# Optimization experiments

Measured on AMD Instinct MI355X. Metric: run time of the kernel, lower is better.

Reference implementation:

```python
import jax, jax.numpy as jnp
import numpy as np

N = 100000   # nodes
E = 1600000  # edges
D = 128      # input feature dim
H1, H2 = 128, 128    # GCN hidden sizes
M1, M2 = 256, 128    # MLP hidden sizes
BN_EPS = 1e-5


def setup_inputs() -> dict:
    key = jax.random.key(0)
    ks = jax.random.split(key, 20)
    x = jax.random.normal(ks[0], (N, D), dtype=jnp.float32)
    edge_index = jax.random.randint(ks[1], (2, E), 0, N, dtype=jnp.int32)

    def lin(k, fi, fo):
        s = 1.0 / np.sqrt(fi)
        return jax.random.uniform(k, (fi, fo), jnp.float32, -s, s)

    inp = {"x": x, "edge_index": edge_index}
    inp["Wg1"] = lin(ks[2], D, H1);  inp["bg1"] = jnp.zeros((H1,), jnp.float32)
    inp["g1"]  = jnp.ones((H1,), jnp.float32); inp["be1"] = jnp.zeros((H1,), jnp.float32)
    inp["Wg2"] = lin(ks[3], H1, H2); inp["bg2"] = jnp.zeros((H2,), jnp.float32)
    inp["g2"]  = jnp.ones((H2,), jnp.float32); inp["be2"] = jnp.zeros((H2,), jnp.float32)
    inp["Wm1"] = lin(ks[4], H2, M1); inp["bm1"] = jnp.zeros((M1,), jnp.float32)
    inp["g3"]  = jnp.ones((M1,), jnp.float32); inp["be3"] = jnp.zeros((M1,), jnp.float32)
    inp["Wm2"] = lin(ks[5], M1, M2); inp["bm2"] = jnp.zeros((M2,), jnp.float32)
    inp["g4"]  = jnp.ones((M2,), jnp.float32); inp["be4"] = jnp.zeros((M2,), jnp.float32)
    inp["Wo"]  = lin(ks[6], M2, 1);  inp["bo"]  = jnp.zeros((1,), jnp.float32)
    return inp


def batch_norm(x, gamma, beta):
    # training-mode BatchNorm1d over the node/batch axis, biased variance
    mean = jnp.mean(x, axis=0)
    var = jnp.mean((x - mean) ** 2, axis=0)
    return (x - mean) * jax.lax.rsqrt(var + BN_EPS) * gamma + beta


def gcn_conv(x, src, dst, W, b):
    # PyG GCNConv: add self-loops, sym-normalize, aggregate (xW) over edges
    h = x @ W                                              # [N, F_out]
    deg = jnp.zeros((N,), x.dtype).at[dst].add(1.0) + 1.0  # in-degree + self-loop
    dinv = jax.lax.rsqrt(deg)
    coef = (dinv[src] * dinv[dst])[:, None]                # [E, 1]
    agg = jax.ops.segment_sum(h[src] * coef, dst, num_segments=N)
    agg = agg + h * (dinv * dinv)[:, None]                 # self-loop term
    return agg + b


def reference(x, edge_index, Wg1, bg1, g1, be1, Wg2, bg2, g2, be2,
              Wm1, bm1, g3, be3, Wm2, bm2, g4, be4, Wo, bo):
    src, dst = edge_index[0], edge_index[1]
    # GCN blocks: relu(dropout(bn(conv(x)))); dropout is identity in eval
    h = jax.nn.relu(batch_norm(gcn_conv(x, src, dst, Wg1, bg1), g1, be1))
    h = jax.nn.relu(batch_norm(gcn_conv(h, src, dst, Wg2, bg2), g2, be2))
    # MLP blocks
    h = jax.nn.relu(batch_norm(h @ Wm1 + bm1, g3, be3))
    h = jax.nn.relu(batch_norm(h @ Wm2 + bm2, g4, be4))
    return jax.nn.sigmoid(h @ Wo + bo)
```

## Files before the change

kernel.cpp:

```cpp
#include <hip/hip_runtime.h>
#include <hip/hip_bf16.h>
#include <math.h>


typedef __attribute__((ext_vector_type(8))) short bf16x8;
typedef __attribute__((ext_vector_type(4))) float f32x4;

__device__ inline void split_bf16(float x, ushort& h, ushort& l) {
    union { float f; unsigned u; } a; a.f = x;
    unsigned r = (a.u + 0x7FFFu + ((a.u >> 16) & 1u)) >> 16;
    h = (ushort)r;
    union { unsigned u; float f; } hb; hb.u = r << 16;
    float lo = x - hb.f;
    union { float f; unsigned u; } b; b.f = lo;
    unsigned r2 = (b.u + 0x7FFFu + ((b.u >> 16) & 1u)) >> 16;
    l = (ushort)r2;
}

__global__ void degree_kernel(const int* __restrict__ dst, int* __restrict__ deg, int E) {
    int i = blockIdx.x * blockDim.x + threadIdx.x;
    if (i < E) atomicAdd(&deg[dst[i]], 1);
}

__global__ void dinv_kernel(const int* __restrict__ deg, float* __restrict__ dinv, int N) {
    int i = blockIdx.x * blockDim.x + threadIdx.x;
    if (i < N) dinv[i] = rsqrtf((float)(deg[i] + 1));
}

__global__ void blocksum_kernel(const int* __restrict__ deg, int* __restrict__ bsum, int N) {
    __shared__ int sh[256];
    int tid = threadIdx.x;
    int base = blockIdx.x * 1024 + tid * 4;
    int s = 0;
    #pragma unroll
    for (int j = 0; j < 4; ++j) { int idx = base + j; if (idx < N) s += deg[idx]; }
    sh[tid] = s; __syncthreads();
    for (int off = 128; off > 0; off >>= 1) {
        if (tid < off) sh[tid] += sh[tid + off];
        __syncthreads();
    }
    if (tid == 0) bsum[blockIdx.x] = sh[0];
}

__global__ void scan_bsum_kernel(int* bsum, int nb) {
    if (threadIdx.x == 0 && blockIdx.x == 0) {
        int run = 0;
        for (int i = 0; i < nb; ++i) { int v = bsum[i]; bsum[i] = run; run += v; }
    }
}

__global__ void scanwrite_kernel(const int* __restrict__ deg, const int* __restrict__ bsumex,
                                 int* __restrict__ row_ptr, int* __restrict__ cursor,
                                 int N, int Etot) {
    __shared__ int sh[256];
    int tid = threadIdx.x;
    int base = blockIdx.x * 1024 + tid * 4;
    int v[4]; int tsum = 0;
    #pragma unroll
    for (int j = 0; j < 4; ++j) { int idx = base + j; v[j] = (idx < N) ? deg[idx] : 0; tsum += v[j]; }
    sh[tid] = tsum; __syncthreads();
    for (int off = 1; off < 256; off <<= 1) {
        int x = (tid >= off) ? sh[tid - off] : 0;
        __syncthreads();
        sh[tid] += x;
        __syncthreads();
    }
    int run = sh[tid] - tsum + bsumex[blockIdx.x];
    #pragma unroll
    for (int j = 0; j < 4; ++j) {
        int idx = base + j;
        if (idx < N) { row_ptr[idx] = run; cursor[idx] = run; }
        run += v[j];
    }
    if (blockIdx.x == 0 && tid == 0) row_ptr[N] = Etot;
}

__global__ void scatter_kernel(const int* __restrict__ src, const int* __restrict__ dst,
                               int* __restrict__ cursor, int* __restrict__ edge_src, int E) {
    int i = blockIdx.x * blockDim.x + threadIdx.x;
    if (i < E) {
        int d = dst[i];
        int pos = atomicAdd(&cursor[d], 1);
        edge_src[pos] = src[i];
    }
}

__global__ void wsplit_kernel(const float* __restrict__ W, ushort* __restrict__ Wh,
                              ushort* __restrict__ Wl, int K, int FO) {
    int t = blockIdx.x * 256 + threadIdx.x;
    if (t >= K * FO) return;
    int j   = t & 7;
    int ci  = (t >> 3) & 127;
    int rest = t >> 10;
    int nkg = K >> 3;
    int kg  = rest % nkg;
    int cb  = rest / nkg;
    float w = W[(size_t)(kg * 8 + j) * FO + cb * 128 + ci];
    ushort h, l; split_bf16(w, h, l);
    Wh[t] = h; Wl[t] = l;
}

#define AIDX(kg, r, j) ((kg) * 1032 + (r) * 8 + (j))

template<bool ACT>
__global__ __launch_bounds__(256)
void gemm_mfma_kernel(const float* __restrict__ A, const ushort* __restrict__ W2h,
                      const ushort* __restrict__ W2l, float* __restrict__ C,
                      int nrows, int K, int FO,
                      const float* __restrict__ scale, const float* __restrict__ shift)
{
    __shared__ ushort AsH[4 * 1032 + 8];
    __shared__ ushort AsL[4 * 1032 + 8];
    const int tid  = threadIdx.x;
    const int lane = tid & 63;
    const int wid  = tid >> 6;
    const int wm   = wid & 1, wn = wid >> 1;
    const int row0 = blockIdx.x * 128;
    const int cb   = blockIdx.y;
    const int c0   = cb * 128;
    const int nkg  = K >> 3;
    const int l15  = lane & 15;
    const int l4   = lane >> 4;

    f32x4 zero = {0.f, 0.f, 0.f, 0.f};
    f32x4 acc[4][4];
    #pragma unroll
    for (int m = 0; m < 4; ++m)
        #pragma unroll
        for (int n = 0; n < 4; ++n) acc[m][n] = zero;

    for (int k0 = 0; k0 < K; k0 += 32) {
        #pragma unroll
        for (int p = 0; p < 4; ++p) {
            int q  = p * 256 + tid;
            int r  = q >> 3;
            int kq = (q & 7) * 4;
            int gr = row0 + r;
            float4 v = make_float4(0.f, 0.f, 0.f, 0.f);
            if (gr < nrows) {
                v = *(const float4*)&A[(size_t)gr * K + k0 + kq];
                if (ACT) {
                    float4 sc = *(const float4*)&scale[k0 + kq];
                    float4 sf = *(const float4*)&shift[k0 + kq];
                    v.x = fmaxf(fmaf(v.x, sc.x, sf.x), 0.f);
                    v.y = fmaxf(fmaf(v.y, sc.y, sf.y), 0.f);
                    v.z = fmaxf(fmaf(v.z, sc.z, sf.z), 0.f);
                    v.w = fmaxf(fmaf(v.w, sc.w, sf.w), 0.f);
                }
            }
            ushort h[4], l[4];
            split_bf16(v.x, h[0], l[0]); split_bf16(v.y, h[1], l[1]);
            split_bf16(v.z, h[2], l[2]); split_bf16(v.w, h[3], l[3]);
            int idx = AIDX(kq >> 3, r, kq & 7);
            union { uint2 u; ushort s[4]; } ph, pl;
            ph.s[0] = h[0]; ph.s[1] = h[1]; ph.s[2] = h[2]; ph.s[3] = h[3];
            pl.s[0] = l[0]; pl.s[1] = l[1]; pl.s[2] = l[2]; pl.s[3] = l[3];
            *(uint2*)&AsH[idx] = ph.u;
            *(uint2*)&AsL[idx] = pl.u;
        }
        __syncthreads();

        const int kgbase = k0 >> 3;
        bf16x8 bh[4], bl[4];
        #pragma unroll
        for (int n = 0; n < 4; ++n) {
            int ci = wn * 64 + n * 16 + l15;
            size_t off = (((size_t)(cb * nkg + kgbase + l4)) * 128 + ci) * 8;
            bh[n] = *(const bf16x8*)&W2h[off];
            bl[n] = *(const bf16x8*)&W2l[off];
        }
        bf16x8 ah[4], al[4];
        #pragma unroll
        for (int m = 0; m < 4; ++m) {
            int idx = AIDX(l4, wm * 64 + m * 16 + l15, 0);
            ah[m] = *(const bf16x8*)&AsH[idx];
            al[m] = *(const bf16x8*)&AsL[idx];
        }
        #pragma unroll
        for (int m = 0; m < 4; ++m)
            #pragma unroll
            for (int n = 0; n < 4; ++n) {
                acc[m][n] = __builtin_amdgcn_mfma_f32_16x16x32_bf16(ah[m], bh[n], acc[m][n], 0, 0, 0);
                acc[m][n] = __builtin_amdgcn_mfma_f32_16x16x32_bf16(ah[m], bl[n], acc[m][n], 0, 0, 0);
                acc[m][n] = __builtin_amdgcn_mfma_f32_16x16x32_bf16(al[m], bh[n], acc[m][n], 0, 0, 0);
            }
        __syncthreads();
    }

    #pragma unroll
    for (int m = 0; m < 4; ++m) {
        int rbase = row0 + wm * 64 + m * 16 + l4 * 4;
        #pragma unroll
        for (int r = 0; r < 4; ++r) {
            int gr = rbase + r;
            if (gr < nrows) {
                #pragma unroll
                for (int n = 0; n < 4; ++n) {
                    int gc = c0 + wn * 64 + n * 16 + l15;
                    C[(size_t)gr * FO + gc] = acc[m][n][r];
                }
            }
        }
    }
}

__global__ void agg_kernel(const float* __restrict__ T, float* __restrict__ Aout,
                           const float* __restrict__ dinv,
                           const int* __restrict__ row_ptr, const int* __restrict__ edge_src,
                           int nrows)
{
    int gw = (blockIdx.x * blockDim.x + threadIdx.x) >> 6;
    int lane = threadIdx.x & 63;
    int nw = (gridDim.x * blockDim.x) >> 6;
    int c = lane * 2;
    for (int i = gw; i < nrows; i += nw) {
        float di = dinv[i];
        int e0 = row_ptr[i], e1 = row_ptr[i + 1];
        float ax = 0.f, ay = 0.f;
        for (int ch = e0; ch < e1; ch += 64) {
            int rem = e1 - ch;
            int es = i; float w = 0.f;
            if (lane < rem) { es = edge_src[ch + lane]; w = dinv[es]; }
            int cnt = min(rem, 64);
            int rcnt = (cnt + 3) & ~3;
            for (int j = 0; j < rcnt; j += 4) {
                int   s0 = __shfl(es, j),     s1 = __shfl(es, j + 1);
                int   s2 = __shfl(es, j + 2), s3 = __shfl(es, j + 3);
                float w0 = __shfl(w, j),      w1 = __shfl(w, j + 1);
                float w2 = __shfl(w, j + 2),  w3 = __shfl(w, j + 3);
                float2 v0 = *(const float2*)&T[(size_t)s0 * 128 + c];
                float2 v1 = *(const float2*)&T[(size_t)s1 * 128 + c];
                float2 v2 = *(const float2*)&T[(size_t)s2 * 128 + c];
                float2 v3 = *(const float2*)&T[(size_t)s3 * 128 + c];
                ax = fmaf(w0, v0.x, ax); ay = fmaf(w0, v0.y, ay);
                ax = fmaf(w1, v1.x, ax); ay = fmaf(w1, v1.y, ay);
                ax = fmaf(w2, v2.x, ax); ay = fmaf(w2, v2.y, ay);
                ax = fmaf(w3, v3.x, ax); ay = fmaf(w3, v3.y, ay);
            }
        }
        float2 self = *(const float2*)&T[(size_t)i * 128 + c];
        float2 o;
        o.x = fmaf(di, ax, di * di * self.x);
        o.y = fmaf(di, ay, di * di * self.y);
        *(float2*)&Aout[(size_t)i * 128 + c] = o;
    }
}

__global__ void colstats_kernel(const float* __restrict__ X, int nrows, int F, int rpb,
                                float* __restrict__ colsum, float* __restrict__ colsq)
{
    __shared__ float ss[256], sq[256];
    int tid = threadIdx.x;
    int c = tid & (F - 1);
    int roff = tid / F;
    int rstep = 256 / F;
    int r0 = blockIdx.x * rpb;
    int r1 = min(nrows, r0 + rpb);
    float s = 0.f, q = 0.f;
    for (int r = r0 + roff; r < r1; r += rstep) {
        float v = X[(size_t)r * F + c];
        s += v; q += v * v;
    }
    ss[tid] = s; sq[tid] = q;
    __syncthreads();
    if (tid < F) {
        float S = ss[tid], Q = sq[tid];
        for (int k = tid + F; k < 256; k += F) { S += ss[k]; Q += sq[k]; }
        atomicAdd(&colsum[tid], S);
        atomicAdd(&colsq[tid], Q);
    }
}

__global__ void bnparam_kernel(const float* __restrict__ colsum, const float* __restrict__ colsq,
                               const float* __restrict__ g, const float* __restrict__ be,
                               float* __restrict__ scale, float* __restrict__ shift,
                               int F, float invN)
{
    int c = blockIdx.x * blockDim.x + threadIdx.x;
    if (c < F) {
        float mean = colsum[c] * invN;
        float var = colsq[c] * invN - mean * mean;
        float rs = rsqrtf(var + 1e-5f);
        float sc = g[c] * rs;
        scale[c] = sc;
        shift[c] = be[c] - mean * sc;
    }
}

__global__ void final_kernel(const float* __restrict__ A, const float* __restrict__ Wo,
                             const float* __restrict__ bo,
                             const float* __restrict__ scale, const float* __restrict__ shift,
                             float* __restrict__ out, int nrows)
{
    int gw = (blockIdx.x * blockDim.x + threadIdx.x) >> 6;
    int lane = threadIdx.x & 63;
    int nw = (gridDim.x * blockDim.x) >> 6;
    int c = lane * 2;
    float2 w = *(const float2*)&Wo[c];
    float2 sc = *(const float2*)&scale[c];
    float2 sf = *(const float2*)&shift[c];
    float bias = bo[0];
    for (int i = gw; i < nrows; i += nw) {
        float2 v = *(const float2*)&A[(size_t)i * 128 + c];
        float x = fmaxf(fmaf(v.x, sc.x, sf.x), 0.f) * w.x
                + fmaxf(fmaf(v.y, sc.y, sf.y), 0.f) * w.y;
        #pragma unroll
        for (int off = 32; off > 0; off >>= 1) x += __shfl_down(x, off);
        if (lane == 0) out[i] = 1.f / (1.f + expf(-(x + bias)));
    }
}

extern "C" void kernel_launch(void* const* d_in, const int* in_sizes, int n_in,
                              void* d_out, int out_size, void* d_ws, size_t ws_size,
                              hipStream_t stream)
{
    const float* x   = (const float*)d_in[0];
    const int* ei    = (const int*)d_in[1];
    const float* Wg1 = (const float*)d_in[2];
    const float* g1  = (const float*)d_in[4];
    const float* be1 = (const float*)d_in[5];
    const float* Wg2 = (const float*)d_in[6];
    const float* g2  = (const float*)d_in[8];
    const float* be2 = (const float*)d_in[9];
    const float* Wm1 = (const float*)d_in[10];
    const float* g3  = (const float*)d_in[12];
    const float* be3 = (const float*)d_in[13];
    const float* Wm2 = (const float*)d_in[14];
    const float* g4  = (const float*)d_in[16];
    const float* be4 = (const float*)d_in[17];
    const float* Wo  = (const float*)d_in[18];
    const float* bo  = (const float*)d_in[19];

    const int N = in_sizes[0] / 128;
    const int E = in_sizes[1] / 2;
    const int* srcv = ei;
    const int* dstv = ei + E;

    char* p = (char*)d_ws;
    auto alloc = [&](size_t bytes) { void* r = (void*)p; p += (bytes + 255) & ~(size_t)255; return r; };
    float* T       = (float*)alloc((size_t)N * 256 * 4);
    float* Abuf    = (float*)alloc((size_t)N * 128 * 4);
    int*   deg     = (int*)alloc((size_t)N * 4);
    float* dinv    = (float*)alloc((size_t)N * 4);
    int*   row_ptr = (int*)alloc((size_t)(N + 1) * 4);
    int*   cursor  = (int*)alloc((size_t)N * 4);
    int*   edge_src= (int*)alloc((size_t)E * 4);
    int*   bsum    = (int*)alloc(4096);
    float* colsum  = (float*)alloc(512 * 4);
    float* colsq   = colsum + 256;
    float* scale   = (float*)alloc(256 * 4);
    float* shift   = (float*)alloc(256 * 4);
    ushort* W2h    = (ushort*)alloc(32768 * 2);
    ushort* W2l    = (ushort*)alloc(32768 * 2);

    const int rpb = (N + 255) / 256;
    const float invN = 1.f / (float)N;

    hipMemsetAsync(deg, 0, (size_t)N * 4, stream);
    degree_kernel<<<(E + 255) / 256, 256, 0, stream>>>(dstv, deg, E);
    dinv_kernel<<<(N + 255) / 256, 256, 0, stream>>>(deg, dinv, N);
    int nb = (N + 1023) / 1024;
    blocksum_kernel<<<nb, 256, 0, stream>>>(deg, bsum, N);
    scan_bsum_kernel<<<1, 64, 0, stream>>>(bsum, nb);
    scanwrite_kernel<<<nb, 256, 0, stream>>>(deg, bsum, row_ptr, cursor, N, E);
    scatter_kernel<<<(E + 255) / 256, 256, 0, stream>>>(srcv, dstv, cursor, edge_src, E);

    const int gx = (N + 127) / 128;
    dim3 gemm_g(gx, 1);
    dim3 gemm_g2(gx, 2);

    wsplit_kernel<<<(128 * 128 + 255) / 256, 256, 0, stream>>>(Wg1, W2h, W2l, 128, 128);
    gemm_mfma_kernel<false><<<gemm_g, 256, 0, stream>>>(x, W2h, W2l, T, N, 128, 128, nullptr, nullptr);
    agg_kernel<<<2048, 256, 0, stream>>>(T, Abuf, dinv, row_ptr, edge_src, N);
    hipMemsetAsync(colsum, 0, 512 * 4, stream);
    colstats_kernel<<<256, 256, 0, stream>>>(Abuf, N, 128, rpb, colsum, colsq);
    bnparam_kernel<<<1, 256, 0, stream>>>(colsum, colsq, g1, be1, scale, shift, 128, invN);

    wsplit_kernel<<<(128 * 128 + 255) / 256, 256, 0, stream>>>(Wg2, W2h, W2l, 128, 128);
    gemm_mfma_kernel<true><<<gemm_g, 256, 0, stream>>>(Abuf, W2h, W2l, T, N, 128, 128, scale, shift);
    agg_kernel<<<2048, 256, 0, stream>>>(T, Abuf, dinv, row_ptr, edge_src, N);
    hipMemsetAsync(colsum, 0, 512 * 4, stream);
    colstats_kernel<<<256, 256, 0, stream>>>(Abuf, N, 128, rpb, colsum, colsq);
    bnparam_kernel<<<1, 256, 0, stream>>>(colsum, colsq, g2, be2, scale, shift, 128, invN);

    wsplit_kernel<<<(128 * 256 + 255) / 256, 256, 0, stream>>>(Wm1, W2h, W2l, 128, 256);
    gemm_mfma_kernel<true><<<gemm_g2, 256, 0, stream>>>(Abuf, W2h, W2l, T, N, 128, 256, scale, shift);
    hipMemsetAsync(colsum, 0, 512 * 4, stream);
    colstats_kernel<<<256, 256, 0, stream>>>(T, N, 256, rpb, colsum, colsq);
    bnparam_kernel<<<1, 256, 0, stream>>>(colsum, colsq, g3, be3, scale, shift, 256, invN);

    wsplit_kernel<<<(256 * 128 + 255) / 256, 256, 0, stream>>>(Wm2, W2h, W2l, 256, 128);
    gemm_mfma_kernel<true><<<gemm_g, 256, 0, stream>>>(T, W2h, W2l, Abuf, N, 256, 128, scale, shift);
    hipMemsetAsync(colsum, 0, 512 * 4, stream);
    colstats_kernel<<<256, 256, 0, stream>>>(Abuf, N, 128, rpb, colsum, colsq);
    bnparam_kernel<<<1, 256, 0, stream>>>(colsum, colsq, g4, be4, scale, shift, 128, invN);

    final_kernel<<<1024, 256, 0, stream>>>(Abuf, Wo, bo, scale, shift, (float*)d_out, N);
}
```

Baseline: 1.027 ms.

## Pre-split activations into MFMA-ready bf16 blobs, load via global_load_lds

```diff
diff --git a/kernel.cpp b/kernel.cpp
--- a/kernel.cpp
+++ b/kernel.cpp
@@ -6,15 +6,21 @@
 typedef __attribute__((ext_vector_type(8))) short bf16x8;
 typedef __attribute__((ext_vector_type(4))) float f32x4;
 
-__device__ inline void split_bf16(float x, ushort& h, ushort& l) {
-    union { float f; unsigned u; } a; a.f = x;
-    unsigned r = (a.u + 0x7FFFu + ((a.u >> 16) & 1u)) >> 16;
-    h = (ushort)r;
-    union { unsigned u; float f; } hb; hb.u = r << 16;
-    float lo = x - hb.f;
-    union { float f; unsigned u; } b; b.f = lo;
-    unsigned r2 = (b.u + 0x7FFFu + ((b.u >> 16) & 1u)) >> 16;
-    l = (ushort)r2;
+__device__ inline void split2(float x, ushort& h, ushort& l) {
+    unsigned u = __float_as_uint(x);
+    h = (ushort)(u >> 16);
+    float hb = __uint_as_float(u & 0xFFFF0000u);
+    float lo = x - hb;
+    unsigned b = __float_as_uint(lo);
+    l = (ushort)((b + 0x7FFFu + ((b >> 16) & 1u)) >> 16);
+}
+
+__device__ inline void gload_lds16(const void* g, void* l) {
+#if defined(__HIP_DEVICE_COMPILE__)
+    __builtin_amdgcn_global_load_lds(
+        (const __attribute__((address_space(1))) unsigned int*)g,
+        (__attribute__((address_space(3))) unsigned int*)l, 16, 0, 0);
+#endif
 }
 
 __global__ void degree_kernel(const int* __restrict__ dst, int* __restrict__ deg, int E) {
@@ -76,49 +82,83 @@
 }
 
 __global__ void scatter_kernel(const int* __restrict__ src, const int* __restrict__ dst,
-                               int* __restrict__ cursor, int* __restrict__ edge_src, int E) {
+                               const float* __restrict__ dinv,
+                               int* __restrict__ cursor, uint2* __restrict__ esw, int E) {
     int i = blockIdx.x * blockDim.x + threadIdx.x;
     if (i < E) {
         int d = dst[i];
+        int s = src[i];
         int pos = atomicAdd(&cursor[d], 1);
-        edge_src[pos] = src[i];
+        esw[pos] = make_uint2((unsigned)s, __float_as_uint(dinv[s]));
     }
 }
 
 __global__ void wsplit_kernel(const float* __restrict__ W, ushort* __restrict__ Wh,
-                              ushort* __restrict__ Wl, int K, int FO) {
+                              ushort* __restrict__ Wl, int FO) {
     int t = blockIdx.x * 256 + threadIdx.x;
-    if (t >= K * FO) return;
+    if (t >= 128 * FO) return;
     int j   = t & 7;
     int ci  = (t >> 3) & 127;
     int rest = t >> 10;
-    int nkg = K >> 3;
-    int kg  = rest % nkg;
-    int cb  = rest / nkg;
+    int kg  = rest & 15;
+    int cb  = rest >> 4;
     float w = W[(size_t)(kg * 8 + j) * FO + cb * 128 + ci];
-    ushort h, l; split_bf16(w, h, l);
+    ushort h, l; split2(w, h, l);
     Wh[t] = h; Wl[t] = l;
 }
-
-#define AIDX(kg, r, j) ((kg) * 1032 + (r) * 8 + (j))
 
 template<bool ACT>
 __global__ __launch_bounds__(256)
-void gemm_mfma_kernel(const float* __restrict__ A, const ushort* __restrict__ W2h,
+void actsplit_kernel(const float* __restrict__ X, char* __restrict__ A2,
+                     const float* __restrict__ scale, const float* __restrict__ shift,
+                     int nrows)
+{
+    int t = blockIdx.x * 256 + threadIdx.x;
+    int r = t & 127;
+    int kg = (t >> 7) & 3;
+    int kstep = (t >> 9) & 3;
+    int rowtile = t >> 11;
+    int gr = rowtile * 128 + r;
+    int k = kstep * 32 + kg * 8;
+    float4 v0 = make_float4(0.f, 0.f, 0.f, 0.f), v1 = v0;
+    if (gr < nrows) {
+        v0 = *(const float4*)&X[(size_t)gr * 128 + k];
+        v1 = *(const float4*)&X[(size_t)gr * 128 + k + 4];
+        if (ACT) {
+            float4 sc0 = *(const float4*)&scale[k],     sf0 = *(const float4*)&shift[k];
+            float4 sc1 = *(const float4*)&scale[k + 4], sf1 = *(const float4*)&shift[k + 4];
+            v0.x = fmaxf(fmaf(v0.x, sc0.x, sf0.x), 0.f);
+            v0.y = fmaxf(fmaf(v0.y, sc0.y, sf0.y), 0.f);
+            v0.z = fmaxf(fmaf(v0.z, sc0.z, sf0.z), 0.f);
+            v0.w = fmaxf(fmaf(v0.w, sc0.w, sf0.w), 0.f);
+            v1.x = fmaxf(fmaf(v1.x, sc1.x, sf1.x), 0.f);
+            v1.y = fmaxf(fmaf(v1.y, sc1.y, sf1.y), 0.f);
+            v1.z = fmaxf(fmaf(v1.z, sc1.z, sf1.z), 0.f);
+            v1.w = fmaxf(fmaf(v1.w, sc1.w, sf1.w), 0.f);
+        }
+    }
+    union { uint4 u; ushort s[8]; } ph, pl;
+    split2(v0.x, ph.s[0], pl.s[0]); split2(v0.y, ph.s[1], pl.s[1]);
+    split2(v0.z, ph.s[2], pl.s[2]); split2(v0.w, ph.s[3], pl.s[3]);
+    split2(v1.x, ph.s[4], pl.s[4]); split2(v1.y, ph.s[5], pl.s[5]);
+    split2(v1.z, ph.s[6], pl.s[6]); split2(v1.w, ph.s[7], pl.s[7]);
+    char* base = A2 + ((size_t)(rowtile * 4 + kstep) * 16384) + kg * 2048 + r * 16;
+    *(uint4*)base          = ph.u;
+    *(uint4*)(base + 8192) = pl.u;
+}
+
+template<bool ACC>
+__global__ __launch_bounds__(256)
+void gemm_mfma_kernel(const char* __restrict__ A2, const ushort* __restrict__ W2h,
                       const ushort* __restrict__ W2l, float* __restrict__ C,
-                      int nrows, int K, int FO,
-                      const float* __restrict__ scale, const float* __restrict__ shift)
-{
-    __shared__ ushort AsH[4 * 1032 + 8];
-    __shared__ ushort AsL[4 * 1032 + 8];
+                      int nrows, int cbW)
+{
+    __shared__ char lds[16384];
     const int tid  = threadIdx.x;
     const int lane = tid & 63;
     const int wid  = tid >> 6;
     const int wm   = wid & 1, wn = wid >> 1;
     const int row0 = blockIdx.x * 128;
-    const int cb   = blockIdx.y;
-    const int c0   = cb * 128;
-    const int nkg  = K >> 3;
     const int l15  = lane & 15;
     const int l4   = lane >> 4;
 
@@ -129,52 +169,29 @@
         #pragma unroll
         for (int n = 0; n < 4; ++n) acc[m][n] = zero;
 
-    for (int k0 = 0; k0 < K; k0 += 32) {
+    const char* blob = A2 + ((size_t)blockIdx.x * 4) * 16384;
+
+    for (int kstep = 0; kstep < 4; ++kstep) {
+        const char* src = blob + (size_t)kstep * 16384;
         #pragma unroll
         for (int p = 0; p < 4; ++p) {
-            int q  = p * 256 + tid;
-            int r  = q >> 3;
-            int kq = (q & 7) * 4;
-            int gr = row0 + r;
-            float4 v = make_float4(0.f, 0.f, 0.f, 0.f);
-            if (gr < nrows) {
-                v = *(const float4*)&A[(size_t)gr * K + k0 + kq];
-                if (ACT) {
-                    float4 sc = *(const float4*)&scale[k0 + kq];
-                    float4 sf = *(const float4*)&shift[k0 + kq];
-                    v.x = fmaxf(fmaf(v.x, sc.x, sf.x), 0.f);
-                    v.y = fmaxf(fmaf(v.y, sc.y, sf.y), 0.f);
-                    v.z = fmaxf(fmaf(v.z, sc.z, sf.z), 0.f);
-                    v.w = fmaxf(fmaf(v.w, sc.w, sf.w), 0.f);
-                }
-            }
-            ushort h[4], l[4];
-            split_bf16(v.x, h[0], l[0]); split_bf16(v.y, h[1], l[1]);
-            split_bf16(v.z, h[2], l[2]); split_bf16(v.w, h[3], l[3]);
-            int idx = AIDX(kq >> 3, r, kq & 7);
-            union { uint2 u; ushort s[4]; } ph, pl;
-            ph.s[0] = h[0]; ph.s[1] = h[1]; ph.s[2] = h[2]; ph.s[3] = h[3];
-            pl.s[0] = l[0]; pl.s[1] = l[1]; pl.s[2] = l[2]; pl.s[3] = l[3];
-            *(uint2*)&AsH[idx] = ph.u;
-            *(uint2*)&AsL[idx] = pl.u;
-        }
-        __syncthreads();
-
-        const int kgbase = k0 >> 3;
+            gload_lds16(src + (((p * 4 + wid) * 64 + lane) * 16), &lds[(p * 4 + wid) * 1024]);
+        }
         bf16x8 bh[4], bl[4];
         #pragma unroll
         for (int n = 0; n < 4; ++n) {
             int ci = wn * 64 + n * 16 + l15;
-            size_t off = (((size_t)(cb * nkg + kgbase + l4)) * 128 + ci) * 8;
+            size_t off = (((size_t)(cbW * 16 + kstep * 4 + l4)) * 128 + ci) * 8;
             bh[n] = *(const bf16x8*)&W2h[off];
             bl[n] = *(const bf16x8*)&W2l[off];
         }
+        __syncthreads();
         bf16x8 ah[4], al[4];
         #pragma unroll
         for (int m = 0; m < 4; ++m) {
-            int idx = AIDX(l4, wm * 64 + m * 16 + l15, 0);
-            ah[m] = *(const bf16x8*)&AsH[idx];
-            al[m] = *(const bf16x8*)&AsL[idx];
+            int o = l4 * 2048 + (wm * 64 + m * 16 + l15) * 16;
+            ah[m] = *(const bf16x8*)&lds[o];
+            al[m] = *(const bf16x8*)&lds[o + 8192];
         }
         #pragma unroll
         for (int m = 0; m < 4; ++m)
@@ -196,8 +213,10 @@
             if (gr < nrows) {
                 #pragma unroll
                 for (int n = 0; n < 4; ++n) {
-                    int gc = c0 + wn * 64 + n * 16 + l15;
-                    C[(size_t)gr * FO + gc] = acc[m][n][r];
+                    int gc = wn * 64 + n * 16 + l15;
+                    size_t idx = (size_t)gr * 128 + gc;
+                    if (ACC) C[idx] += acc[m][n][r];
+                    else     C[idx]  = acc[m][n][r];
                 }
             }
         }
@@ -206,7 +225,7 @@
 
 __global__ void agg_kernel(const float* __restrict__ T, float* __restrict__ Aout,
                            const float* __restrict__ dinv,
-                           const int* __restrict__ row_ptr, const int* __restrict__ edge_src,
+                           const int* __restrict__ row_ptr, const uint2* __restrict__ esw,
                            int nrows)
 {
     int gw = (blockIdx.x * blockDim.x + threadIdx.x) >> 6;
@@ -215,57 +234,59 @@
     int c = lane * 2;
     for (int i = gw; i < nrows; i += nw) {
         float di = dinv[i];
-        int e0 = row_ptr[i], e1 = row_ptr[i + 1];
-        float ax = 0.f, ay = 0.f;
-        for (int ch = e0; ch < e1; ch += 64) {
-            int rem = e1 - ch;
-            int es = i; float w = 0.f;
-            if (lane < rem) { es = edge_src[ch + lane]; w = dinv[es]; }
-            int cnt = min(rem, 64);
-            int rcnt = (cnt + 3) & ~3;
-            for (int j = 0; j < rcnt; j += 4) {
-                int   s0 = __shfl(es, j),     s1 = __shfl(es, j + 1);
-                int   s2 = __shfl(es, j + 2), s3 = __shfl(es, j + 3);
-                float w0 = __shfl(w, j),      w1 = __shfl(w, j + 1);
-                float w2 = __shfl(w, j + 2),  w3 = __shfl(w, j + 3);
-                float2 v0 = *(const float2*)&T[(size_t)s0 * 128 + c];
-                float2 v1 = *(const float2*)&T[(size_t)s1 * 128 + c];
-                float2 v2 = *(const float2*)&T[(size_t)s2 * 128 + c];
-                float2 v3 = *(const float2*)&T[(size_t)s3 * 128 + c];
-                ax = fmaf(w0, v0.x, ax); ay = fmaf(w0, v0.y, ay);
-                ax = fmaf(w1, v1.x, ax); ay = fmaf(w1, v1.y, ay);
-                ax = fmaf(w2, v2.x, ax); ay = fmaf(w2, v2.y, ay);
-                ax = fmaf(w3, v3.x, ax); ay = fmaf(w3, v3.y, ay);
-            }
-        }
-        float2 self = *(const float2*)&T[(size_t)i * 128 + c];
+        int e0 = __builtin_amdgcn_readfirstlane(row_ptr[i]);
+        int e1 = __builtin_amdgcn_readfirstlane(row_ptr[i + 1]);
+        float ax0 = 0.f, ay0 = 0.f, ax1 = 0.f, ay1 = 0.f;
+        int e = e0;
+        int eq = e0 + ((e1 - e0) & ~3);
+        for (; e < eq; e += 4) {
+            uint2 p0 = esw[e],     p1 = esw[e + 1];
+            uint2 p2 = esw[e + 2], p3 = esw[e + 3];
+            float2 v0 = *(const float2*)&T[((size_t)p0.x << 7) + c];
+            float2 v1 = *(const float2*)&T[((size_t)p1.x << 7) + c];
+            float2 v2 = *(const float2*)&T[((size_t)p2.x << 7) + c];
+            float2 v3 = *(const float2*)&T[((size_t)p3.x << 7) + c];
+            float w0 = __uint_as_float(p0.y), w1 = __uint_as_float(p1.y);
+            float w2 = __uint_as_float(p2.y), w3 = __uint_as_float(p3.y);
+            ax0 = fmaf(w0, v0.x, ax0); ay0 = fmaf(w0, v0.y, ay0);
+            ax1 = fmaf(w1, v1.x, ax1); ay1 = fmaf(w1, v1.y, ay1);
+            ax0 = fmaf(w2, v2.x, ax0); ay0 = fmaf(w2, v2.y, ay0);
+            ax1 = fmaf(w3, v3.x, ax1); ay1 = fmaf(w3, v3.y, ay1);
+        }
+        for (; e < e1; ++e) {
+            uint2 p = esw[e];
+            float w = __uint_as_float(p.y);
+            float2 v = *(const float2*)&T[((size_t)p.x << 7) + c];
+            ax0 = fmaf(w, v.x, ax0); ay0 = fmaf(w, v.y, ay0);
+        }
+        float ax = ax0 + ax1, ay = ay0 + ay1;
+        float2 self = *(const float2*)&T[((size_t)i << 7) + c];
         float2 o;
         o.x = fmaf(di, ax, di * di * self.x);
         o.y = fmaf(di, ay, di * di * self.y);
-        *(float2*)&Aout[(size_t)i * 128 + c] = o;
-    }
-}
-
-__global__ void colstats_kernel(const float* __restrict__ X, int nrows, int F, int rpb,
+        *(float2*)&Aout[((size_t)i << 7) + c] = o;
+    }
+}
+
+__global__ void colstats_kernel(const float* __restrict__ X, int nrows, int rpb,
                                 float* __restrict__ colsum, float* __restrict__ colsq)
 {
     __shared__ float ss[256], sq[256];
     int tid = threadIdx.x;
-    int c = tid & (F - 1);
-    int roff = tid / F;
-    int rstep = 256 / F;
+    int c = tid & 127;
+    int roff = tid >> 7;
     int r0 = blockIdx.x * rpb;
     int r1 = min(nrows, r0 + rpb);
     float s = 0.f, q = 0.f;
-    for (int r = r0 + roff; r < r1; r += rstep) {
-        float v = X[(size_t)r * F + c];
+    for (int r = r0 + roff; r < r1; r += 2) {
+        float v = X[(size_t)r * 128 + c];
         s += v; q += v * v;
     }
     ss[tid] = s; sq[tid] = q;
     __syncthreads();
-    if (tid < F) {
-        float S = ss[tid], Q = sq[tid];
-        for (int k = tid + F; k < 256; k += F) { S += ss[k]; Q += sq[k]; }
+    if (tid < 128) {
+        float S = ss[tid] + ss[tid + 128];
+        float Q = sq[tid] + sq[tid + 128];
         atomicAdd(&colsum[tid], S);
         atomicAdd(&colsq[tid], Q);
     }
@@ -274,10 +295,10 @@
 __global__ void bnparam_kernel(const float* __restrict__ colsum, const float* __restrict__ colsq,
                                const float* __restrict__ g, const float* __restrict__ be,
                                float* __restrict__ scale, float* __restrict__ shift,
-                               int F, float invN)
-{
-    int c = blockIdx.x * blockDim.x + threadIdx.x;
-    if (c < F) {
+                               float invN)
+{
+    int c = threadIdx.x;
+    if (c < 128) {
         float mean = colsum[c] * invN;
         float var = colsq[c] * invN - mean * mean;
         float rs = rsqrtf(var + 1e-5f);
@@ -335,65 +356,83 @@
     const int E = in_sizes[1] / 2;
     const int* srcv = ei;
     const int* dstv = ei + E;
+    const int rowtiles = (N + 127) / 128;
+    const size_t blobsz = (size_t)rowtiles * 4 * 16384;
 
     char* p = (char*)d_ws;
     auto alloc = [&](size_t bytes) { void* r = (void*)p; p += (bytes + 255) & ~(size_t)255; return r; };
-    float* T       = (float*)alloc((size_t)N * 256 * 4);
-    float* Abuf    = (float*)alloc((size_t)N * 128 * 4);
+    float* buf1    = (float*)alloc((size_t)N * 128 * 4);
+    char*  buf2    = (char*)alloc(blobsz);
+    char*  buf3    = (char*)alloc(blobsz);
     int*   deg     = (int*)alloc((size_t)N * 4);
     float* dinv    = (float*)alloc((size_t)N * 4);
     int*   row_ptr = (int*)alloc((size_t)(N + 1) * 4);
     int*   cursor  = (int*)alloc((size_t)N * 4);
-    int*   edge_src= (int*)alloc((size_t)E * 4);
+    uint2* esw     = (uint2*)alloc((size_t)(E + 8) * 8);
     int*   bsum    = (int*)alloc(4096);
     float* colsum  = (float*)alloc(512 * 4);
-    float* colsq   = colsum + 256;
+    float* colsq   = colsum + 128;
     float* scale   = (float*)alloc(256 * 4);
     float* shift   = (float*)alloc(256 * 4);
     ushort* W2h    = (ushort*)alloc(32768 * 2);
     ushort* W2l    = (ushort*)alloc(32768 * 2);
 
+    float* Abuf = (float*)buf2;
+    float* C4   = (float*)buf3;
     const int rpb = (N + 255) / 256;
     const float invN = 1.f / (float)N;
-
-    hipMemsetAsync(deg, 0, (size_t)N * 4, stream);
+    const int as_blocks = rowtiles * 8;
+
+    (void)hipMemsetAsync(deg, 0, (size_t)N * 4, stream);
     degree_kernel<<<(E + 255) / 256, 256, 0, stream>>>(dstv, deg, E);
     dinv_kernel<<<(N + 255) / 256, 256, 0, stream>>>(deg, dinv, N);
     int nb = (N + 1023) / 1024;
     blocksum_kernel<<<nb, 256, 0, stream>>>(deg, bsum, N);
     scan_bsum_kernel<<<1, 64, 0, stream>>>(bsum, nb);
     scanwrite_kernel<<<nb, 256, 0, stream>>>(deg, bsum, row_ptr, cursor, N, E);
-    scatter_kernel<<<(E + 255) / 256, 256, 0, stream>>>(srcv, dstv, cursor, edge_src, E);
-
-    const int gx = (N + 127) / 128;
-    dim3 gemm_g(gx, 1);
-    dim3 gemm_g2(gx, 2);
-
-    wsplit_kernel<<<(128 * 128 + 255) / 256, 256, 0, stream>>>(Wg1, W2h, W2l, 128, 128);
-    gemm_mfma_kernel<false><<<gemm_g, 256, 0, stream>>>(x, W2h, W2l, T, N, 128, 128, nullptr, nullptr);
-    agg_kernel<<<2048, 256, 0, stream>>>(T, Abuf, dinv, row_ptr, edge_src, N);
-    hipMemsetAsync(colsum, 0, 512 * 4, stream);
-    colstats_kernel<<<256, 256, 0, stream>>>(Abuf, N, 128, rpb, colsum, colsq);
-    bnparam_kernel<<<1, 256, 0, stream>>>(colsum, colsq, g1, be1, scale, shift, 128, invN);
-
-    wsplit_kernel<<<(128 * 128 + 255) / 256, 256, 0, stream>>>(Wg2, W2h, W2l, 128, 128);
-    gemm_mfma_kernel<true><<<gemm_g, 256, 0, stream>>>(Abuf, W2h, W2l, T, N, 128, 128, scale, shift);
-    agg_kernel<<<2048, 256, 0, stream>>>(T, Abuf, dinv, row_ptr, edge_src, N);
-    hipMemsetAsync(colsum, 0, 512 * 4, stream);
-    colstats_kernel<<<256, 256, 0, stream>>>(Abuf, N, 128, rpb, colsum, colsq);
-    bnparam_kernel<<<1, 256, 0, stream>>>(colsum, colsq, g2, be2, scale, shift, 128, invN);
-
-    wsplit_kernel<<<(128 * 256 + 255) / 256, 256, 0, stream>>>(Wm1, W2h, W2l, 128, 256);
-    gemm_mfma_kernel<true><<<gemm_g2, 256, 0, stream>>>(Abuf, W2h, W2l, T, N, 128, 256, scale, shift);
-    hipMemsetAsync(colsum, 0, 512 * 4, stream);
-    colstats_kernel<<<256, 256, 0, stream>>>(T, N, 256, rpb, colsum, colsq);
-    bnparam_kernel<<<1, 256, 0, stream>>>(colsum, colsq, g3, be3, scale, shift, 256, invN);
-
-    wsplit_kernel<<<(256 * 128 + 255) / 256, 256, 0, stream>>>(Wm2, W2h, W2l, 256, 128);
-    gemm_mfma_kernel<true><<<gemm_g, 256, 0, stream>>>(T, W2h, W2l, Abuf, N, 256, 128, scale, shift);
-    hipMemsetAsync(colsum, 0, 512 * 4, stream);
-    colstats_kernel<<<256, 256, 0, stream>>>(Abuf, N, 128, rpb, colsum, colsq);
-    bnparam_kernel<<<1, 256, 0, stream>>>(colsum, colsq, g4, be4, scale, shift, 128, invN);
-
-    final_kernel<<<1024, 256, 0, stream>>>(Abuf, Wo, bo, scale, shift, (float*)d_out, N);
-}
+    scatter_kernel<<<(E + 255) / 256, 256, 0, stream>>>(srcv, dstv, dinv, cursor, esw, E);
+
+    dim3 gg(rowtiles, 1);
+
+    wsplit_kernel<<<64, 256, 0, stream>>>(Wg1, W2h, W2l, 128);
+    actsplit_kernel<false><<<as_blocks, 256, 0, stream>>>(x, buf3, nullptr, nullptr, N);
+    gemm_mfma_kernel<false><<<gg, 256, 0, stream>>>(buf3, W2h, W2l, buf1, N, 0);
+    agg_kernel<<<2048, 256, 0, stream>>>(buf1, Abuf, dinv, row_ptr, esw, N);
+    (void)hipMemsetAsync(colsum, 0, 256 * 4, stream);
+    colstats_kernel<<<256, 256, 0, stream>>>(Abuf, N, rpb, colsum, colsq);
+    bnparam_kernel<<<1, 128, 0, stream>>>(colsum, colsq, g1, be1, scale, shift, invN);
+
+    wsplit_kernel<<<64, 256, 0, stream>>>(Wg2, W2h, W2l, 128);
+    actsplit_kernel<true><<<as_blocks, 256, 0, stream>>>(Abuf, buf3, scale, shift, N);
+    gemm_mfma_kernel<false><<<gg, 256, 0, stream>>>(buf3, W2h, W2l, buf1, N, 0);
+    agg_kernel<<<2048, 256, 0, stream>>>(buf1, Abuf, dinv, row_ptr, esw, N);
+    (void)hipMemsetAsync(colsum, 0, 256 * 4, stream);
+    colstats_kernel<<<256, 256, 0, stream>>>(Abuf, N, rpb, colsum, colsq);
+    bnparam_kernel<<<1, 128, 0, stream>>>(colsum, colsq, g2, be2, scale, shift, invN);
+
+    actsplit_kernel<true><<<as_blocks, 256, 0, stream>>>(Abuf, buf3, scale, shift, N);
+    wsplit_kernel<<<128, 256, 0, stream>>>(Wm1, W2h, W2l, 256);
+
+    gemm_mfma_kernel<false><<<gg, 256, 0, stream>>>(buf3, W2h, W2l, buf1, N, 0);
+    (void)hipMemsetAsync(colsum, 0, 256 * 4, stream);
+    colstats_kernel<<<256, 256, 0, stream>>>(buf1, N, rpb, colsum, colsq);
+    bnparam_kernel<<<1, 128, 0, stream>>>(colsum, colsq, g3, be3, scale, shift, invN);
+    actsplit_kernel<true><<<as_blocks, 256, 0, stream>>>(buf1, buf2, scale, shift, N);
+
+    gemm_mfma_kernel<false><<<gg, 256, 0, stream>>>(buf3, W2h, W2l, buf1, N, 1);
+    (void)hipMemsetAsync(colsum, 0, 256 * 4, stream);
+    colstats_kernel<<<256, 256, 0, stream>>>(buf1, N, rpb, colsum, colsq);
+    bnparam_kernel<<<1, 128, 0, stream>>>(colsum, colsq, g3 + 128, be3 + 128, scale, shift, invN);
+
+    wsplit_kernel<<<64, 256, 0, stream>>>(Wm2, W2h, W2l, 128);
+    gemm_mfma_kernel<false><<<gg, 256, 0, stream>>>(buf2, W2h, W2l, C4, N, 0);
+
+    actsplit_kernel<true><<<as_blocks, 256, 0, stream>>>(buf1, buf2, scale, shift, N);
+    wsplit_kernel<<<64, 256, 0, stream>>>(Wm2 + 128 * 128, W2h, W2l, 128);
+    gemm_mfma_kernel<true><<<gg, 256, 0, stream>>>(buf2, W2h, W2l, C4, N, 0);
+
+    (void)hipMemsetAsync(colsum, 0, 256 * 4, stream);
+    colstats_kernel<<<256, 256, 0, stream>>>(C4, N, rpb, colsum, colsq);
+    bnparam_kernel<<<1, 128, 0, stream>>>(colsum, colsq, g4, be4, scale, shift, invN);
+    final_kernel<<<1024, 256, 0, stream>>>(C4, Wo, bo, scale, shift, (float*)d_out, N);
+}
```

New measurement: 1.069 ms. +4.1%, slower.
